# Kernel tuning notes

Hardware: AMD Instinct MI355X
Metric: run time of the kernel (lower is better)

## Reference

```python
import jax, jax.numpy as jnp
import numpy as np

B, N, IN_DIM, OUT_DIM, HEADS = 4, 2048, 128, 32, 8
NEG_SLOPE = 0.2


def setup_inputs() -> dict:
    key = jax.random.key(0)
    k_x, k_adj, k_w, k_as, k_ad = jax.random.split(key, 5)
    x = jax.random.normal(k_x, (B, N, IN_DIM), dtype=jnp.float32)
    adj = jax.random.randint(k_adj, (B, N, N), 0, 2).astype(jnp.float32)
    # xavier_uniform bounds
    lim_w = float(np.sqrt(6.0 / (IN_DIM + OUT_DIM)))
    lim_a = float(np.sqrt(6.0 / (OUT_DIM + 1)))
    W = jax.random.uniform(k_w, (HEADS, IN_DIM, OUT_DIM), dtype=jnp.float32, minval=-lim_w, maxval=lim_w)
    a_src = jax.random.uniform(k_as, (HEADS, OUT_DIM), dtype=jnp.float32, minval=-lim_a, maxval=lim_a)
    a_dst = jax.random.uniform(k_ad, (HEADS, OUT_DIM), dtype=jnp.float32, minval=-lim_a, maxval=lim_a)
    return {"x": x, "adj": adj, "W": W, "a_src": a_src, "a_dst": a_dst}


def reference(x, adj, W, a_src, a_dst):
    # Wh: [B,H,N,O]
    Wh = jnp.einsum('bnf,hfo->bhno', x, W)
    alpha_src = jnp.einsum('bhno,ho->bhn', Wh, a_src)  # [B,H,N]
    alpha_dst = jnp.einsum('bhno,ho->bhn', Wh, a_dst)  # [B,H,N]
    # additive scores e[b,h,i,j] = alpha_src[b,h,i] + alpha_dst[b,h,j]
    e = alpha_src[..., :, None] + alpha_dst[..., None, :]
    e = jnp.where(e >= 0, e, NEG_SLOPE * e)  # leaky_relu(0.2)
    n = adj.shape[-1]
    eye = jnp.eye(n, dtype=adj.dtype)
    mask = (adj + eye[None] > 0)[:, None, :, :]  # [B,1,N,N]
    e = jnp.where(mask, e, -jnp.inf)
    attn = jax.nn.softmax(e, axis=-1)  # every row has self-loop -> finite
    out = jnp.einsum('bhij,bhjo->bhio', attn, Wh)  # [B,H,N,O]
    b = x.shape[0]
    out = jnp.transpose(out, (0, 2, 1, 3)).reshape(b, n, HEADS * OUT_DIM)
    return jax.nn.relu(out)
```

## Files before the change

kernel.cpp:

```cpp
#include <hip/hip_runtime.h>
#include <math.h>

#define BB 4
#define NSZ 2048
#define FDIM 128
#define ODIM 32
#define HH 8

typedef short short8 __attribute__((ext_vector_type(8)));
typedef float f32x4 __attribute__((ext_vector_type(4)));

#define WS_EAP  0
#define WS_EBP  131072
#define WS_ADJB 262144
#define WS_WHF  786432

__device__ __forceinline__ unsigned bfbits(float f) {
    unsigned u = __builtin_bit_cast(unsigned, f);
    return u + 0x7fffu + ((u >> 16) & 1u);
}
__device__ __forceinline__ unsigned bfpack(float a, float b) {
    return __builtin_amdgcn_perm(bfbits(b), bfbits(a), 0x07060302);
}

__global__ __launch_bounds__(256) void k_prep(const float* __restrict__ x,
                                              const float* __restrict__ adj,
                                              const float* __restrict__ W,
                                              const float* __restrict__ a_src,
                                              const float* __restrict__ a_dst,
                                              unsigned* __restrict__ adjb,
                                              int4* __restrict__ whf,
                                              float2* __restrict__ eap,
                                              float2* __restrict__ ebp) {
    __shared__ float wsl[FDIM * 33];
    __shared__ unsigned short wlds[64][33];
    int t = threadIdx.x;

    if (blockIdx.x < 16384) {
        int g = blockIdx.x * 256 + t;
        int l = g & 7;
        int word = g >> 3;
        int wk = word & 63;
        int row = word >> 6;
        int i = row & (NSZ - 1);
        const float4 v = *(const float4*)&adj[(size_t)row * NSZ + wk * 32 + l * 4];
        unsigned m = 0;
        if (v.x > 0.f) m |= 1u << (l * 4 + 0);
        if (v.y > 0.f) m |= 1u << (l * 4 + 1);
        if (v.z > 0.f) m |= 1u << (l * 4 + 2);
        if (v.w > 0.f) m |= 1u << (l * 4 + 3);
        m |= (unsigned)__shfl_xor((int)m, 1);
        m |= (unsigned)__shfl_xor((int)m, 2);
        m |= (unsigned)__shfl_xor((int)m, 4);
        if (l == 0) {
            int jb = i - wk * 32;
            if (jb >= 0 && jb < 32) m |= 1u << jb;
            adjb[word] = m;
        }
        return;
    }

    int bidx = blockIdx.x - 16384;
    int b = bidx >> 8;
    int h = (bidx >> 5) & 7;
    int nt = bidx & 31;
    int n0 = nt * 64;
    int w = t >> 6, lane = t & 63;
    int col = lane & 15, quad = lane >> 4;

#pragma unroll
    for (int m = 0; m < 16; m++) {
        int idx = t + m * 256;
        wsl[(idx >> 5) * 33 + (idx & 31)] = W[(size_t)h * (FDIM * ODIM) + idx];
    }

    const float* xp = x + ((size_t)(b * NSZ) + n0 + w * 16 + col) * FDIM + quad * 8;
    int4 afr[4];
#pragma unroll
    for (int kt = 0; kt < 4; kt++) {
        float4 xa = *(const float4*)(xp + kt * 32);
        float4 xb = *(const float4*)(xp + kt * 32 + 4);
        afr[kt] = make_int4((int)bfpack(xa.x, xa.y), (int)bfpack(xa.z, xa.w),
                            (int)bfpack(xb.x, xb.y), (int)bfpack(xb.z, xb.w));
    }
    __syncthreads();

    f32x4 alo = {0.f, 0.f, 0.f, 0.f};
    f32x4 ahi = {0.f, 0.f, 0.f, 0.f};
#pragma unroll
    for (int kt = 0; kt < 4; kt++) {
        short8 a8 = __builtin_bit_cast(short8, afr[kt]);
#pragma unroll
        for (int ot = 0; ot < 2; ot++) {
            unsigned d[4];
#pragma unroll
            for (int jp = 0; jp < 4; jp++) {
                float lo = wsl[(kt * 32 + quad * 8 + 2 * jp) * 33 + ot * 16 + col];
                float hi = wsl[(kt * 32 + quad * 8 + 2 * jp + 1) * 33 + ot * 16 + col];
                d[jp] = bfpack(lo, hi);
            }
            int4 bf = make_int4((int)d[0], (int)d[1], (int)d[2], (int)d[3]);
            if (ot == 0)
                alo = __builtin_amdgcn_mfma_f32_16x16x32_bf16(a8,
                        __builtin_bit_cast(short8, bf), alo, 0, 0, 0);
            else
                ahi = __builtin_amdgcn_mfma_f32_16x16x32_bf16(a8,
                        __builtin_bit_cast(short8, bf), ahi, 0, 0, 0);
        }
    }

    float as0 = a_src[h * ODIM + col], as1 = a_src[h * ODIM + 16 + col];
    float ad0 = a_dst[h * ODIM + col], ad1 = a_dst[h * ODIM + 16 + col];
#pragma unroll
    for (int r = 0; r < 4; r++) {
        float pa = alo[r] * as0 + ahi[r] * as1;
        float pb = alo[r] * ad0 + ahi[r] * ad1;
#pragma unroll
        for (int mk = 1; mk <= 8; mk <<= 1) {
            pa += __shfl_xor(pa, mk);
            pb += __shfl_xor(pb, mk);
        }
        if (col == 0) {
            size_t idx = (size_t)(b * HH + h) * NSZ + n0 + w * 16 + quad * 4 + r;
            eap[idx] = make_float2(__expf(pa - 8.f), __expf(0.2f * pa - 8.f));
            ebp[idx] = make_float2(__expf(pb - 8.f), __expf(0.2f * pb - 8.f));
        }
    }

#pragma unroll
    for (int r = 0; r < 4; r++) {
        wlds[w * 16 + quad * 4 + r][col]      = (unsigned short)(bfbits(alo[r]) >> 16);
        wlds[w * 16 + quad * 4 + r][col + 16] = (unsigned short)(bfbits(ahi[r]) >> 16);
    }
    __syncthreads();
    int jl = w >> 1, ot = w & 1;
    unsigned d[4];
#pragma unroll
    for (int jp = 0; jp < 4; jp++) {
        unsigned lo = wlds[jl * 32 + quad * 8 + 2 * jp][ot * 16 + col];
        unsigned hi = wlds[jl * 32 + quad * 8 + 2 * jp + 1][ot * 16 + col];
        d[jp] = (hi << 16) | lo;
    }
    int fragid = ((b * HH + h) * 64 + nt * 2 + jl) * 2 + ot;
    whf[(size_t)fragid * 64 + lane] = make_int4((int)d[0], (int)d[1], (int)d[2], (int)d[3]);
}

__device__ __forceinline__ int4 pfrag(float eaa, float eab, const float4& l0,
                                      const float4& l1, const float4& l2,
                                      const float4& l3, unsigned w,
                                      const unsigned (*__restrict__ mlut)[2]) {
    float p0 = fmaxf(eaa * l0.x, eab * l0.y);
    float p1 = fmaxf(eaa * l0.z, eab * l0.w);
    float p2 = fmaxf(eaa * l1.x, eab * l1.y);
    float p3 = fmaxf(eaa * l1.z, eab * l1.w);
    float p4 = fmaxf(eaa * l2.x, eab * l2.y);
    float p5 = fmaxf(eaa * l2.z, eab * l2.w);
    float p6 = fmaxf(eaa * l3.x, eab * l3.y);
    float p7 = fmaxf(eaa * l3.z, eab * l3.w);
    unsigned u0 = __builtin_bit_cast(unsigned, p0) + 0x8000u;
    unsigned u1 = __builtin_bit_cast(unsigned, p1) + 0x8000u;
    unsigned u2 = __builtin_bit_cast(unsigned, p2) + 0x8000u;
    unsigned u3 = __builtin_bit_cast(unsigned, p3) + 0x8000u;
    unsigned u4 = __builtin_bit_cast(unsigned, p4) + 0x8000u;
    unsigned u5 = __builtin_bit_cast(unsigned, p5) + 0x8000u;
    unsigned u6 = __builtin_bit_cast(unsigned, p6) + 0x8000u;
    unsigned u7 = __builtin_bit_cast(unsigned, p7) + 0x8000u;
    unsigned d0 = __builtin_amdgcn_perm(u1, u0, 0x07060302);
    unsigned d1 = __builtin_amdgcn_perm(u3, u2, 0x07060302);
    unsigned d2 = __builtin_amdgcn_perm(u5, u4, 0x07060302);
    unsigned d3 = __builtin_amdgcn_perm(u7, u6, 0x07060302);
    const unsigned* mA = mlut[w & 15];
    const unsigned* mB = mlut[(w >> 4) & 15];
    return make_int4((int)(d0 & mA[0]), (int)(d1 & mA[1]),
                     (int)(d2 & mB[0]), (int)(d3 & mB[1]));
}

__global__ __launch_bounds__(256) void k_gat(const int4* __restrict__ whf,
                                             const float2* __restrict__ eap,
                                             const float2* __restrict__ ebp,
                                             const unsigned* __restrict__ adjb,
                                             float* __restrict__ out) {
    __shared__ float ebl[4096];
    __shared__ float comb[2][24][64];
    __shared__ unsigned mlut[16][2];

    int t = threadIdx.x;
    int u = blockIdx.x;
    int unit = (u & 7) * 128 + (u >> 3);
    int b = unit >> 8;
    int h = (unit >> 5) & 7;
    int i0 = (unit & 31) * 64;
    int wave = t >> 6, lane = t & 63;
    int it = wave & 1, jh = wave >> 1;
    int col = lane & 15, quad = lane >> 4, qsh = quad * 8;
    size_t bh = (size_t)(b * HH + h);

    if (t < 16) {
        mlut[t][0] = ((t & 1) ? 0x0000FFFFu : 0u) | ((t & 2) ? 0xFFFF0000u : 0u);
        mlut[t][1] = ((t & 4) ? 0x0000FFFFu : 0u) | ((t & 8) ? 0xFFFF0000u : 0u);
    }

    const float4* ebg = (const float4*)(ebp + bh * NSZ);
#pragma unroll
    for (int k = 0; k < 4; k++) ((float4*)ebl)[t + k * 256] = ebg[t + k * 256];

    int iw = i0 + it * 32;
    float2 ea0 = eap[bh * NSZ + iw + col];
    float2 ea1 = eap[bh * NSZ + iw + 16 + col];
    const uint4* mp0 = (const uint4*)(adjb + ((size_t)(b * NSZ) + iw + col) * 64) + jh * 8;
    const uint4* mp1 = (const uint4*)(adjb + ((size_t)(b * NSZ) + iw + 16 + col) * 64) + jh * 8;
    const int4* bfp = whf + bh * 8192 + lane;

    f32x4 a00 = {0.f,0.f,0.f,0.f}, a01 = {0.f,0.f,0.f,0.f}, a0d = {0.f,0.f,0.f,0.f};
    f32x4 a10 = {0.f,0.f,0.f,0.f}, a11 = {0.f,0.f,0.f,0.f}, a1d = {0.f,0.f,0.f,0.f};
    const int4 onesv = make_int4(0x3F803F80, 0x3F803F80, 0x3F803F80, 0x3F803F80);
    short8 bones = __builtin_bit_cast(short8, onesv);

    __syncthreads();

    for (int jt4 = 0; jt4 < 8; jt4++) {
        uint4 m0 = mp0[jt4];
        uint4 m1 = mp1[jt4];
        unsigned m0a[4] = {m0.x, m0.y, m0.z, m0.w};
        unsigned m1a[4] = {m1.x, m1.y, m1.z, m1.w};
#pragma unroll
        for (int q = 0; q < 4; q++) {
            int jt = jh * 32 + jt4 * 4 + q;
            const float4* el = (const float4*)&ebl[(jt * 32 + qsh) * 2];
            float4 l0 = el[0], l1 = el[1], l2 = el[2], l3 = el[3];
            int4 blo = bfp[jt * 128];
            int4 bhi = bfp[jt * 128 + 64];
            int4 f0 = pfrag(ea0.x, ea0.y, l0, l1, l2, l3, m0a[q] >> qsh, mlut);
            int4 f1 = pfrag(ea1.x, ea1.y, l0, l1, l2, l3, m1a[q] >> qsh, mlut);
            short8 af0 = __builtin_bit_cast(short8, f0);
            short8 af1 = __builtin_bit_cast(short8, f1);
            short8 b0 = __builtin_bit_cast(short8, blo);
            short8 b1 = __builtin_bit_cast(short8, bhi);
            a00 = __builtin_amdgcn_mfma_f32_16x16x32_bf16(af0, b0, a00, 0, 0, 0);
            a01 = __builtin_amdgcn_mfma_f32_16x16x32_bf16(af0, b1, a01, 0, 0, 0);
            a0d = __builtin_amdgcn_mfma_f32_16x16x32_bf16(af0, bones, a0d, 0, 0, 0);
            a10 = __builtin_amdgcn_mfma_f32_16x16x32_bf16(af1, b0, a10, 0, 0, 0);
            a11 = __builtin_amdgcn_mfma_f32_16x16x32_bf16(af1, b1, a11, 0, 0, 0);
            a1d = __builtin_amdgcn_mfma_f32_16x16x32_bf16(af1, bones, a1d, 0, 0, 0);
        }
    }

    if (jh) {
#pragma unroll
        for (int r = 0; r < 4; r++) {
            comb[it][r][lane]      = a00[r];
            comb[it][4 + r][lane]  = a01[r];
            comb[it][8 + r][lane]  = a0d[r];
            comb[it][12 + r][lane] = a10[r];
            comb[it][16 + r][lane] = a11[r];
            comb[it][20 + r][lane] = a1d[r];
        }
    }
    __syncthreads();
    if (jh) return;
#pragma unroll
    for (int r = 0; r < 4; r++) {
        a00[r] += comb[it][r][lane];
        a01[r] += comb[it][4 + r][lane];
        a0d[r] += comb[it][8 + r][lane];
        a10[r] += comb[it][12 + r][lane];
        a11[r] += comb[it][16 + r][lane];
        a1d[r] += comb[it][20 + r][lane];
    }

    float* op = out + ((size_t)(b * NSZ) + iw) * (HH * ODIM) + h * ODIM + col;
#pragma unroll
    for (int r = 0; r < 4; r++) {
        int row = quad * 4 + r;
        float inv0 = 1.0f / a0d[r];
        float inv1 = 1.0f / a1d[r];
        op[(size_t)row * (HH * ODIM)]           = fmaxf(a00[r] * inv0, 0.f);
        op[(size_t)row * (HH * ODIM) + 16]      = fmaxf(a01[r] * inv0, 0.f);
        op[(size_t)(row + 16) * (HH * ODIM)]      = fmaxf(a10[r] * inv1, 0.f);
        op[(size_t)(row + 16) * (HH * ODIM) + 16] = fmaxf(a11[r] * inv1, 0.f);
    }
}

extern "C" void kernel_launch(void* const* d_in, const int* in_sizes, int n_in,
                              void* d_out, int out_size, void* d_ws, size_t ws_size,
                              hipStream_t stream) {
    const float* x     = (const float*)d_in[0];
    const float* adj   = (const float*)d_in[1];
    const float* W     = (const float*)d_in[2];
    const float* a_src = (const float*)d_in[3];
    const float* a_dst = (const float*)d_in[4];
    float* out = (float*)d_out;

    float* ws = (float*)d_ws;
    float2* eap    = (float2*)(ws + WS_EAP);
    float2* ebp    = (float2*)(ws + WS_EBP);
    unsigned* adjb = (unsigned*)(ws + WS_ADJB);
    int4* whf      = (int4*)(ws + WS_WHF);

    k_prep<<<dim3(16384 + 1024), dim3(256), 0, stream>>>(x, adj, W, a_src, a_dst,
                                                         adjb, whf, eap, ebp);
    k_gat<<<dim3(BB * HH * (NSZ / 64)), dim3(256), 0, stream>>>(whf, eap, ebp, adjb, out);
}
```

Before: 137.2 us.

## Split j-range across four waves each covering all 64 rows, compute masks arithmetically

Each wave now handles all 64 query rows (four 16-row fragments) over a quarter of the key range, so every B fragment and every ebl LDS read is reused four times instead of twice. The adjacency mask is built with shifts and perm instead of an LDS lookup table, and the bf16 round-up add is dropped in favour of truncation. Launch bounds request 4 blocks per CU, and a two-stage LDS tree reduction combines the partial sums from the four waves. The cost is more accumulator registers, extra syncs in the reduction, and slightly different bf16 rounding.

```diff
diff --git a/kernel.cpp b/kernel.cpp
--- a/kernel.cpp
+++ b/kernel.cpp
@@ -147,8 +147,7 @@
 
 __device__ __forceinline__ int4 pfrag(float eaa, float eab, const float4& l0,
                                       const float4& l1, const float4& l2,
-                                      const float4& l3, unsigned w,
-                                      const unsigned (*__restrict__ mlut)[2]) {
+                                      const float4& l3, unsigned word, int shb) {
     float p0 = fmaxf(eaa * l0.x, eab * l0.y);
     float p1 = fmaxf(eaa * l0.z, eab * l0.w);
     float p2 = fmaxf(eaa * l1.x, eab * l1.y);
@@ -157,32 +156,31 @@
     float p5 = fmaxf(eaa * l2.z, eab * l2.w);
     float p6 = fmaxf(eaa * l3.x, eab * l3.y);
     float p7 = fmaxf(eaa * l3.z, eab * l3.w);
-    unsigned u0 = __builtin_bit_cast(unsigned, p0) + 0x8000u;
-    unsigned u1 = __builtin_bit_cast(unsigned, p1) + 0x8000u;
-    unsigned u2 = __builtin_bit_cast(unsigned, p2) + 0x8000u;
-    unsigned u3 = __builtin_bit_cast(unsigned, p3) + 0x8000u;
-    unsigned u4 = __builtin_bit_cast(unsigned, p4) + 0x8000u;
-    unsigned u5 = __builtin_bit_cast(unsigned, p5) + 0x8000u;
-    unsigned u6 = __builtin_bit_cast(unsigned, p6) + 0x8000u;
-    unsigned u7 = __builtin_bit_cast(unsigned, p7) + 0x8000u;
-    unsigned d0 = __builtin_amdgcn_perm(u1, u0, 0x07060302);
-    unsigned d1 = __builtin_amdgcn_perm(u3, u2, 0x07060302);
-    unsigned d2 = __builtin_amdgcn_perm(u5, u4, 0x07060302);
-    unsigned d3 = __builtin_amdgcn_perm(u7, u6, 0x07060302);
-    const unsigned* mA = mlut[w & 15];
-    const unsigned* mB = mlut[(w >> 4) & 15];
-    return make_int4((int)(d0 & mA[0]), (int)(d1 & mA[1]),
-                     (int)(d2 & mB[0]), (int)(d3 & mB[1]));
-}
-
-__global__ __launch_bounds__(256) void k_gat(const int4* __restrict__ whf,
-                                             const float2* __restrict__ eap,
-                                             const float2* __restrict__ ebp,
-                                             const unsigned* __restrict__ adjb,
-                                             float* __restrict__ out) {
-    __shared__ float ebl[4096];
-    __shared__ float comb[2][24][64];
-    __shared__ unsigned mlut[16][2];
+    unsigned d0 = __builtin_amdgcn_perm(__builtin_bit_cast(unsigned, p1),
+                                        __builtin_bit_cast(unsigned, p0), 0x07060302);
+    unsigned d1 = __builtin_amdgcn_perm(__builtin_bit_cast(unsigned, p3),
+                                        __builtin_bit_cast(unsigned, p2), 0x07060302);
+    unsigned d2 = __builtin_amdgcn_perm(__builtin_bit_cast(unsigned, p5),
+                                        __builtin_bit_cast(unsigned, p4), 0x07060302);
+    unsigned d3 = __builtin_amdgcn_perm(__builtin_bit_cast(unsigned, p7),
+                                        __builtin_bit_cast(unsigned, p6), 0x07060302);
+    unsigned mk[4];
+#pragma unroll
+    for (int k = 0; k < 4; k++) {
+        int s0 = ((int)(word << (shb - 2 * k))) >> 31;
+        int s1 = ((int)(word << (shb - 2 * k - 1))) >> 31;
+        mk[k] = __builtin_amdgcn_perm((unsigned)s1, (unsigned)s0, 0x07060302);
+    }
+    return make_int4((int)(d0 & mk[0]), (int)(d1 & mk[1]),
+                     (int)(d2 & mk[2]), (int)(d3 & mk[3]));
+}
+
+__global__ __launch_bounds__(256, 4) void k_gat(const int4* __restrict__ whf,
+                                                const float2* __restrict__ eap,
+                                                const float2* __restrict__ ebp,
+                                                const unsigned* __restrict__ adjb,
+                                                float* __restrict__ out) {
+    __shared__ float sbuf[6144];
 
     int t = threadIdx.x;
     int u = blockIdx.x;
@@ -191,94 +189,111 @@
     int h = (unit >> 5) & 7;
     int i0 = (unit & 31) * 64;
     int wave = t >> 6, lane = t & 63;
-    int it = wave & 1, jh = wave >> 1;
     int col = lane & 15, quad = lane >> 4, qsh = quad * 8;
+    int shb = 31 - qsh;
     size_t bh = (size_t)(b * HH + h);
 
-    if (t < 16) {
-        mlut[t][0] = ((t & 1) ? 0x0000FFFFu : 0u) | ((t & 2) ? 0xFFFF0000u : 0u);
-        mlut[t][1] = ((t & 4) ? 0x0000FFFFu : 0u) | ((t & 8) ? 0xFFFF0000u : 0u);
-    }
-
     const float4* ebg = (const float4*)(ebp + bh * NSZ);
 #pragma unroll
-    for (int k = 0; k < 4; k++) ((float4*)ebl)[t + k * 256] = ebg[t + k * 256];
-
-    int iw = i0 + it * 32;
-    float2 ea0 = eap[bh * NSZ + iw + col];
-    float2 ea1 = eap[bh * NSZ + iw + 16 + col];
-    const uint4* mp0 = (const uint4*)(adjb + ((size_t)(b * NSZ) + iw + col) * 64) + jh * 8;
-    const uint4* mp1 = (const uint4*)(adjb + ((size_t)(b * NSZ) + iw + 16 + col) * 64) + jh * 8;
+    for (int k = 0; k < 4; k++) ((float4*)sbuf)[t + k * 256] = ebg[t + k * 256];
+
+    float2 ea[4];
+    const uint4* mp[4];
+#pragma unroll
+    for (int f = 0; f < 4; f++) {
+        ea[f] = eap[bh * NSZ + i0 + f * 16 + col];
+        mp[f] = (const uint4*)(adjb + ((size_t)(b * NSZ) + i0 + f * 16 + col) * 64) + wave * 4;
+    }
     const int4* bfp = whf + bh * 8192 + lane;
 
-    f32x4 a00 = {0.f,0.f,0.f,0.f}, a01 = {0.f,0.f,0.f,0.f}, a0d = {0.f,0.f,0.f,0.f};
-    f32x4 a10 = {0.f,0.f,0.f,0.f}, a11 = {0.f,0.f,0.f,0.f}, a1d = {0.f,0.f,0.f,0.f};
+    f32x4 ac[4][3];
+#pragma unroll
+    for (int f = 0; f < 4; f++)
+#pragma unroll
+        for (int c = 0; c < 3; c++) ac[f][c] = (f32x4){0.f, 0.f, 0.f, 0.f};
     const int4 onesv = make_int4(0x3F803F80, 0x3F803F80, 0x3F803F80, 0x3F803F80);
     short8 bones = __builtin_bit_cast(short8, onesv);
 
     __syncthreads();
 
-    for (int jt4 = 0; jt4 < 8; jt4++) {
-        uint4 m0 = mp0[jt4];
-        uint4 m1 = mp1[jt4];
-        unsigned m0a[4] = {m0.x, m0.y, m0.z, m0.w};
-        unsigned m1a[4] = {m1.x, m1.y, m1.z, m1.w};
+    for (int jt4 = 0; jt4 < 4; jt4++) {
+        uint4 mw[4];
+#pragma unroll
+        for (int f = 0; f < 4; f++) mw[f] = mp[f][jt4];
 #pragma unroll
         for (int q = 0; q < 4; q++) {
-            int jt = jh * 32 + jt4 * 4 + q;
-            const float4* el = (const float4*)&ebl[(jt * 32 + qsh) * 2];
+            int jt = wave * 16 + jt4 * 4 + q;
+            const float4* el = (const float4*)&sbuf[(jt * 32 + qsh) * 2];
             float4 l0 = el[0], l1 = el[1], l2 = el[2], l3 = el[3];
             int4 blo = bfp[jt * 128];
             int4 bhi = bfp[jt * 128 + 64];
-            int4 f0 = pfrag(ea0.x, ea0.y, l0, l1, l2, l3, m0a[q] >> qsh, mlut);
-            int4 f1 = pfrag(ea1.x, ea1.y, l0, l1, l2, l3, m1a[q] >> qsh, mlut);
-            short8 af0 = __builtin_bit_cast(short8, f0);
-            short8 af1 = __builtin_bit_cast(short8, f1);
             short8 b0 = __builtin_bit_cast(short8, blo);
             short8 b1 = __builtin_bit_cast(short8, bhi);
-            a00 = __builtin_amdgcn_mfma_f32_16x16x32_bf16(af0, b0, a00, 0, 0, 0);
-            a01 = __builtin_amdgcn_mfma_f32_16x16x32_bf16(af0, b1, a01, 0, 0, 0);
-            a0d = __builtin_amdgcn_mfma_f32_16x16x32_bf16(af0, bones, a0d, 0, 0, 0);
-            a10 = __builtin_amdgcn_mfma_f32_16x16x32_bf16(af1, b0, a10, 0, 0, 0);
-            a11 = __builtin_amdgcn_mfma_f32_16x16x32_bf16(af1, b1, a11, 0, 0, 0);
-            a1d = __builtin_amdgcn_mfma_f32_16x16x32_bf16(af1, bones, a1d, 0, 0, 0);
-        }
-    }
-
-    if (jh) {
+            unsigned wq[4] = {mw[0].x, mw[1].x, mw[2].x, mw[3].x};
+            if (q == 1) { wq[0] = mw[0].y; wq[1] = mw[1].y; wq[2] = mw[2].y; wq[3] = mw[3].y; }
+            if (q == 2) { wq[0] = mw[0].z; wq[1] = mw[1].z; wq[2] = mw[2].z; wq[3] = mw[3].z; }
+            if (q == 3) { wq[0] = mw[0].w; wq[1] = mw[1].w; wq[2] = mw[2].w; wq[3] = mw[3].w; }
+#pragma unroll
+            for (int f = 0; f < 4; f++) {
+                int4 fr = pfrag(ea[f].x, ea[f].y, l0, l1, l2, l3, wq[f], shb);
+                short8 a8 = __builtin_bit_cast(short8, fr);
+                ac[f][0] = __builtin_amdgcn_mfma_f32_16x16x32_bf16(a8, b0, ac[f][0], 0, 0, 0);
+                ac[f][1] = __builtin_amdgcn_mfma_f32_16x16x32_bf16(a8, b1, ac[f][1], 0, 0, 0);
+                ac[f][2] = __builtin_amdgcn_mfma_f32_16x16x32_bf16(a8, bones, ac[f][2], 0, 0, 0);
+            }
+        }
+    }
+
+    f32x4* reg0 = (f32x4*)&sbuf[0];
+    f32x4* reg1 = (f32x4*)&sbuf[3072];
+    __syncthreads();
+    if (wave >= 2) {
+        f32x4* rg = (wave == 2) ? reg0 : reg1;
+#pragma unroll
+        for (int f = 0; f < 4; f++)
+#pragma unroll
+            for (int c = 0; c < 3; c++) rg[(f * 3 + c) * 64 + lane] = ac[f][c];
+    }
+    __syncthreads();
+    if (wave < 2) {
+        f32x4* rg = (wave == 0) ? reg0 : reg1;
+#pragma unroll
+        for (int f = 0; f < 4; f++)
+#pragma unroll
+            for (int c = 0; c < 3; c++) {
+                f32x4 v = rg[(f * 3 + c) * 64 + lane];
+#pragma unroll
+                for (int r = 0; r < 4; r++) ac[f][c][r] += v[r];
+            }
+    }
+    __syncthreads();
+    if (wave == 1) {
+#pragma unroll
+        for (int f = 0; f < 4; f++)
+#pragma unroll
+            for (int c = 0; c < 3; c++) reg0[(f * 3 + c) * 64 + lane] = ac[f][c];
+    }
+    __syncthreads();
+    if (wave != 0) return;
+#pragma unroll
+    for (int f = 0; f < 4; f++)
+#pragma unroll
+        for (int c = 0; c < 3; c++) {
+            f32x4 v = reg0[(f * 3 + c) * 64 + lane];
+#pragma unroll
+            for (int r = 0; r < 4; r++) ac[f][c][r] += v[r];
+        }
+
+    float* op = out + ((size_t)(b * NSZ) + i0) * (HH * ODIM) + h * ODIM + col;
+#pragma unroll
+    for (int f = 0; f < 4; f++)
 #pragma unroll
         for (int r = 0; r < 4; r++) {
-            comb[it][r][lane]      = a00[r];
-            comb[it][4 + r][lane]  = a01[r];
-            comb[it][8 + r][lane]  = a0d[r];
-            comb[it][12 + r][lane] = a10[r];
-            comb[it][16 + r][lane] = a11[r];
-            comb[it][20 + r][lane] = a1d[r];
-        }
-    }
-    __syncthreads();
-    if (jh) return;
-#pragma unroll
-    for (int r = 0; r < 4; r++) {
-        a00[r] += comb[it][r][lane];
-        a01[r] += comb[it][4 + r][lane];
-        a0d[r] += comb[it][8 + r][lane];
-        a10[r] += comb[it][12 + r][lane];
-        a11[r] += comb[it][16 + r][lane];
-        a1d[r] += comb[it][20 + r][lane];
-    }
-
-    float* op = out + ((size_t)(b * NSZ) + iw) * (HH * ODIM) + h * ODIM + col;
-#pragma unroll
-    for (int r = 0; r < 4; r++) {
-        int row = quad * 4 + r;
-        float inv0 = 1.0f / a0d[r];
-        float inv1 = 1.0f / a1d[r];
-        op[(size_t)row * (HH * ODIM)]           = fmaxf(a00[r] * inv0, 0.f);
-        op[(size_t)row * (HH * ODIM) + 16]      = fmaxf(a01[r] * inv0, 0.f);
-        op[(size_t)(row + 16) * (HH * ODIM)]      = fmaxf(a10[r] * inv1, 0.f);
-        op[(size_t)(row + 16) * (HH * ODIM) + 16] = fmaxf(a11[r] * inv1, 0.f);
-    }
+            int row = f * 16 + quad * 4 + r;
+            float inv = 1.0f / ac[f][2][r];
+            op[(size_t)row * (HH * ODIM)]      = fmaxf(ac[f][0][r] * inv, 0.f);
+            op[(size_t)row * (HH * ODIM) + 16] = fmaxf(ac[f][1][r] * inv, 0.f);
+        }
 }
 
 extern "C" void kernel_launch(void* const* d_in, const int* in_sizes, int n_in,
```

Result: slower. 146.2 us (+6.6%).
